# Performance work log

Measured on AMD Instinct MI355X. Metric: run time of the kernel, lower is better.

The kernel has to match this reference:

```python
import jax, jax.numpy as jnp
import numpy as np

POS_THRES = 0.7
NEG_THRES = 0.3
POS_RATIO = 0.5
N_SAMPLES = 256
FH, FW, STRIDE = 200, 200, 16
RATIOS = (1.0, 2.0)
N_GT = 256
IMG_H = FH * STRIDE
IMG_W = FW * STRIDE
A = FH * FW * len(RATIOS)
N_POS_BUDGET = int(POS_RATIO * N_SAMPLES)


def _make_anchors():
    # centre format [cy, cx, h, w]; one anchor per (cell, ratio)
    ys = (np.arange(FH) + 0.5) * STRIDE
    xs = (np.arange(FW) + 0.5) * STRIDE
    cy, cx = np.meshgrid(ys, xs, indexing='ij')          # [FH, FW]
    hs = np.array([STRIDE * np.sqrt(r) for r in RATIOS])  # [R]
    ws = np.array([STRIDE / np.sqrt(r) for r in RATIOS])
    cy = np.broadcast_to(cy[..., None], (FH, FW, len(RATIOS)))
    cx = np.broadcast_to(cx[..., None], (FH, FW, len(RATIOS)))
    h = np.broadcast_to(hs, (FH, FW, len(RATIOS)))
    w = np.broadcast_to(ws, (FH, FW, len(RATIOS)))
    centre = np.stack([cy, cx, h, w], -1).reshape(-1, 4).astype(np.float32)
    corner = np.stack([centre[:, 0] - centre[:, 2] / 2,
                       centre[:, 1] - centre[:, 3] / 2,
                       centre[:, 0] + centre[:, 2] / 2,
                       centre[:, 1] + centre[:, 3] / 2], -1).astype(np.float32)
    return jnp.asarray(centre), jnp.asarray(corner)


def setup_inputs() -> dict:
    key = jax.random.key(0)
    k1, k2, k3, k4, k5, k6 = jax.random.split(key, 6)
    centre_anchors, corner_anchors = _make_anchors()
    rpn_pred_bnd = jax.random.normal(k1, (1, A, 4), dtype=jnp.float32)
    rpn_pred_class = jax.random.normal(k2, (1, A, 2), dtype=jnp.float32)
    # gt boxes in centre form [cy, cx, h, w], inside the 3200x3200 image
    cy = jax.random.uniform(k3, (N_GT,), minval=200.0, maxval=IMG_H - 200.0)
    cx = jax.random.uniform(k4, (N_GT,), minval=200.0, maxval=IMG_W - 200.0)
    h = jax.random.uniform(k5, (N_GT,), minval=16.0, maxval=300.0)
    w = jax.random.uniform(k6, (N_GT,), minval=16.0, maxval=300.0)
    target_bnds = jnp.stack([cy, cx, h, w], 1).astype(jnp.float32)
    return {"rpn_pred_bnd": rpn_pred_bnd, "rpn_pred_class": rpn_pred_class,
            "target_bnds": target_bnds, "centre_anchors": centre_anchors,
            "corner_anchors": corner_anchors}


def _cxcy_to_corners(b):
    return jnp.stack([b[:, 0] - b[:, 2] / 2, b[:, 1] - b[:, 3] / 2,
                      b[:, 0] + b[:, 2] / 2, b[:, 1] + b[:, 3] / 2], 1)


def _iou(anc, tgt):
    # anc [A,4], tgt [N,4] in corner form [y1,x1,y2,x2] -> IoU [A,N]
    y1 = jnp.maximum(anc[:, None, 0], tgt[None, :, 0])
    x1 = jnp.maximum(anc[:, None, 1], tgt[None, :, 1])
    y2 = jnp.minimum(anc[:, None, 2], tgt[None, :, 2])
    x2 = jnp.minimum(anc[:, None, 3], tgt[None, :, 3])
    inter = jnp.clip(y2 - y1, 0.0) * jnp.clip(x2 - x1, 0.0)
    area_a = (anc[:, 2] - anc[:, 0]) * (anc[:, 3] - anc[:, 1])
    area_t = (tgt[:, 2] - tgt[:, 0]) * (tgt[:, 3] - tgt[:, 1])
    return inter / (area_a[:, None] + area_t[None, :] - inter)


def _subsample(mask, budget, key):
    # keep at most `budget` True entries, chosen uniformly at random (masked rank trick)
    pri = jax.random.uniform(key, mask.shape)
    pri = jnp.where(mask, pri, jnp.inf)
    order = jnp.argsort(pri)
    rank = jnp.zeros(mask.shape[0], dtype=jnp.int32).at[order].set(
        jnp.arange(mask.shape[0], dtype=jnp.int32))
    return mask & (rank < budget)


def reference(rpn_pred_bnd, rpn_pred_class, target_bnds, centre_anchors, corner_anchors):
    skey = jax.random.key(42)
    k_pos, k_neg = jax.random.split(skey)

    corner_targets = _cxcy_to_corners(target_bnds)
    valid = ((corner_anchors[:, 0] >= 0) & (corner_anchors[:, 1] >= 0) &
             (corner_anchors[:, 2] <= IMG_H) & (corner_anchors[:, 3] <= IMG_W))

    iou = _iou(corner_anchors, corner_targets)               # [A, N]
    iou = jnp.where(valid[:, None], iou, -1.0)               # mask invalid anchors out
    anchor_gt_overlap = iou.max(axis=1)                      # best gt per anchor
    anchor_gt_ind = iou.argmax(axis=1)
    gt_best_anchor = iou.argmax(axis=0)                      # best anchor per gt [N]

    labels = jnp.full((A,), -1, dtype=jnp.int32)
    labels = jnp.where(valid & (anchor_gt_overlap < NEG_THRES), 0, labels)
    labels = jnp.where(valid & (anchor_gt_overlap > POS_THRES), 1, labels)
    labels = labels.at[gt_best_anchor].set(1)                # force a positive per gt

    # subsample positives to POS_RATIO * N_SAMPLES
    keep_pos = _subsample(labels == 1, jnp.int32(N_POS_BUDGET), k_pos)
    labels = jnp.where((labels == 1) & ~keep_pos, -1, labels)
    n_pos_kept = jnp.sum(labels == 1).astype(jnp.int32)
    # subsample negatives to fill remaining budget
    keep_neg = _subsample(labels == 0, N_SAMPLES - n_pos_kept, k_neg)
    labels = jnp.where((labels == 0) & ~keep_neg, -1, labels)

    t = target_bnds[anchor_gt_ind]                           # [A,4]
    ty = (t[:, 0] - centre_anchors[:, 0]) / centre_anchors[:, 2]
    tx = (t[:, 1] - centre_anchors[:, 1]) / centre_anchors[:, 3]
    th = jnp.log(t[:, 2] / centre_anchors[:, 2])
    tw = jnp.log(t[:, 3] / centre_anchors[:, 3])
    anchor_targets = jnp.stack([ty, tx, th, tw], 1)

    pb = rpn_pred_bnd[0]                                     # [A,4]
    pc = rpn_pred_class[0]                                   # [A,2]
    posf = (labels == 1).astype(pb.dtype)
    negf = (labels == 0).astype(pb.dtype)
    n_pos = posf.sum()
    n_neg = negf.sum()

    def l1(c):
        return (jnp.abs(pb[:, c] - anchor_targets[:, c]) * posf).sum() / n_pos

    loss_y, loss_x, loss_h, loss_w = l1(0), l1(1), l1(2), l1(3)
    logp = jax.nn.log_softmax(pc, axis=-1)
    loss_pos_class = -(logp[:, 1] * posf).sum() / n_pos
    loss_neg_class = -(logp[:, 0] * negf).sum() / n_neg
    return (loss_x, loss_y, loss_h, loss_w, loss_pos_class, loss_neg_class)
```

## Files before the change

### kernel.cpp

```cpp
#include <hip/hip_runtime.h>
#include <stdint.h>

#pragma clang fp contract(off)

#define A_TOT   80000
#define NGT     256
#define IMGH    3200.0f
#define IMGW    3200.0f
#define NPOSB   128
#define NSAMP   256
#define FW      200
#define NBX     13
#define ANB     157
#define SEGW    512
#define NEG_BIN_MAX 119u
#define SENT (~0ull)
#define SELT 1024
#define SLOTS 16
#define SUBCAP 1024

struct U2 { uint32_t a, b; };

constexpr uint32_t rotl32c(uint32_t x, int d) {
  return (x << d) | (x >> (32 - d));
}

constexpr U2 tf2x32c(uint32_t k0, uint32_t k1, uint32_t x0, uint32_t x1) {
  uint32_t ks2 = k0 ^ k1 ^ 0x1BD11BDAu;
  x0 += k0; x1 += k1;
#define TF_G(r0_, r1_, r2_, r3_)                                   \
  { x0 += x1; x1 = rotl32c(x1, r0_); x1 ^= x0;                     \
    x0 += x1; x1 = rotl32c(x1, r1_); x1 ^= x0;                     \
    x0 += x1; x1 = rotl32c(x1, r2_); x1 ^= x0;                     \
    x0 += x1; x1 = rotl32c(x1, r3_); x1 ^= x0; }
  TF_G(13, 15, 26, 6);  x0 += k1;  x1 += ks2 + 1u;
  TF_G(17, 29, 16, 24); x0 += ks2; x1 += k0 + 2u;
  TF_G(13, 15, 26, 6);  x0 += k0;  x1 += k1 + 3u;
  TF_G(17, 29, 16, 24); x0 += k1;  x1 += ks2 + 4u;
  TF_G(13, 15, 26, 6);  x0 += ks2; x1 += k0 + 5u;
#undef TF_G
  return U2{x0, x1};
}

constexpr U2 KPOS = tf2x32c(0u, 42u, 0u, 0u);
constexpr U2 KNEG = tf2x32c(0u, 42u, 0u, 1u);

__device__ __forceinline__ uint32_t unif_prib(uint32_t k0, uint32_t k1, uint32_t idx) {
  U2 r = tf2x32c(k0, k1, 0u, idx);
  uint32_t w = r.a ^ r.b;
  uint32_t fb = (w >> 9) | 0x3f800000u;
  float pri = __uint_as_float(fb) - 1.0f;
  return __float_as_uint(pri);
}

__device__ __forceinline__ uint32_t binP(uint32_t pbv) {
  float pri = __uint_as_float(pbv);
  uint32_t b = (uint32_t)(pri * 512.0f);
  return b > 511u ? 511u : b;
}
__device__ __forceinline__ uint32_t binN(uint32_t pbv) {
  float pri = __uint_as_float(pbv);
  uint32_t b = (uint32_t)(pri * 65536.0f);
  return b > 511u ? 511u : b;
}

__device__ __forceinline__ float iou_fn(float ay1, float ax1, float ay2, float ax2,
                                        float area_a,
                                        float ty1, float tx1, float ty2, float tx2,
                                        float area_t) {
  float y1 = fmaxf(ay1, ty1);
  float x1 = fmaxf(ax1, tx1);
  float y2 = fminf(ay2, ty2);
  float x2 = fminf(ax2, tx2);
  float ih = y2 - y1; ih = fmaxf(ih, 0.0f);
  float iw = x2 - x1; iw = fmaxf(iw, 0.0f);
  float inter = ih * iw;
  float denom = area_a + area_t - inter;
  return inter / denom;
}

__device__ __forceinline__ uint32_t ord_bits(float v) {
  uint32_t b = __float_as_uint(v);
  return b ^ (((int)b < 0) ? 0xFFFFFFFFu : 0x80000000u);
}

__global__ __launch_bounds__(256)
void k_main(const float* __restrict__ cA, const float* __restrict__ tgt,
            int* __restrict__ labels, int* __restrict__ ind,
            uint32_t* __restrict__ gbest,
            unsigned long long* __restrict__ posSeg,
            unsigned long long* __restrict__ negSeg,
            uint32_t* __restrict__ posCntG, uint32_t* __restrict__ negCntG,
            uint32_t* __restrict__ negTotG) {
  int tid = threadIdx.x;
  int lane = tid & 63, wid = tid >> 6;
  if (blockIdx.x >= ANB) {
    int gt = blockIdx.x - ANB;
    float t0 = tgt[4*gt], t1 = tgt[4*gt+1], t2 = tgt[4*gt+2], t3 = tgt[4*gt+3];
    float ty1 = t0 - t2/2.0f, tx1 = t1 - t3/2.0f;
    float ty2 = t0 + t2/2.0f, tx2 = t1 + t3/2.0f;
    float at = (ty2 - ty1) * (tx2 - tx1);
    const float M = 11.5f;
    int iy0 = (int)floorf((ty1 - M) * 0.0625f - 0.5f) - 1; iy0 = iy0 < 0 ? 0 : iy0;
    int iy1 = (int)ceilf ((ty2 + M) * 0.0625f - 0.5f) + 1; iy1 = iy1 > 199 ? 199 : iy1;
    int ix0 = (int)floorf((tx1 - M) * 0.0625f - 0.5f) - 1; ix0 = ix0 < 0 ? 0 : ix0;
    int ix1 = (int)ceilf ((tx2 + M) * 0.0625f - 0.5f) + 1; ix1 = ix1 > 199 ? 199 : ix1;
    int wx = ix1 - ix0 + 1, wy = iy1 - iy0 + 1;
    int W = wy * wx * 2;
    unsigned long long key = 0ull;
    for (int c = tid; c < W; c += 256) {
      int r = c & 1, q = c >> 1;
      int yy = q / wx, xx = q - yy * wx;
      int a = (((iy0 + yy) * FW + (ix0 + xx)) << 1) | r;
      const float4 av = *reinterpret_cast<const float4*>(&cA[4*a]);
      float ay1 = av.x, ax1 = av.y, ay2 = av.z, ax2 = av.w;
      bool valid = (ay1 >= 0.f) & (ax1 >= 0.f) & (ay2 <= IMGH) & (ax2 <= IMGW);
      float v = -1.0f;
      if (valid) {
        float area_a = (ay2 - ay1) * (ax2 - ax1);
        v = iou_fn(ay1, ax1, ay2, ax2, area_a, ty1, tx1, ty2, tx2, at);
      }
      unsigned long long k2 =
          ((unsigned long long)ord_bits(v) << 32) | (uint32_t)(~(uint32_t)a);
      if (k2 > key) key = k2;
    }
    for (int d = 1; d < 64; d <<= 1) {
      unsigned long long o = __shfl_xor(key, d);
      if (o > key) key = o;
    }
    __shared__ unsigned long long sW[4];
    if (lane == 0) sW[wid] = key;
    __syncthreads();
    if (tid == 0) {
      unsigned long long k = sW[0];
      if (sW[1] > k) k = sW[1];
      if (sW[2] > k) k = sW[2];
      if (sW[3] > k) k = sW[3];
      gbest[gt] = ~(uint32_t)(k & 0xffffffffu);
    }
    return;
  }
  __shared__ float sTy1[NGT], sTx1[NGT], sTy2[NGT], sTx2[NGT], sAr[NGT];
  __shared__ uint32_t sCnt[256], sScan[256], sWs[4], sCur[176], sOrder[NGT];
  __shared__ uint32_t sPosCnt, sNegCnt, sNegTot;
  if (tid == 0) { sPosCnt = 0u; sNegCnt = 0u; sNegTot = 0u; }
  float t0 = tgt[4*tid], t1 = tgt[4*tid+1], t2 = tgt[4*tid+2], t3 = tgt[4*tid+3];
  float gy1 = t0 - t2/2.0f, gx1 = t1 - t3/2.0f;
  float gy2 = t0 + t2/2.0f, gx2 = t1 + t3/2.0f;
  sTy1[tid] = gy1; sTx1[tid] = gx1; sTy2[tid] = gy2; sTx2[tid] = gx2;
  sAr[tid] = (gy2 - gy1) * (gx2 - gx1);
  int gby = (int)(t0 * (1.0f/256.0f)); gby = gby > 12 ? 12 : gby;
  int gbx = (int)(t1 * (1.0f/256.0f)); gbx = gbx > 12 ? 12 : gbx;
  int gb = gby * NBX + gbx;
  sCnt[tid] = 0u;
  __syncthreads();
  atomicAdd(&sCnt[gb], 1u);
  __syncthreads();
  {
    uint32_t incl = sCnt[tid];
#pragma unroll
    for (int d = 1; d < 64; d <<= 1) {
      uint32_t o = __shfl_up(incl, d);
      if (lane >= d) incl += o;
    }
    if (lane == 63) sWs[wid] = incl;
    __syncthreads();
    uint32_t off = 0;
    if (wid > 0) off += sWs[0];
    if (wid > 1) off += sWs[1];
    if (wid > 2) off += sWs[2];
    sScan[tid] = incl + off;
  }
  __syncthreads();
  if (tid < 169) sCur[tid] = (tid == 0) ? 0u : sScan[tid - 1];
  __syncthreads();
  uint32_t pos = atomicAdd(&sCur[gb], 1u);
  sOrder[pos] = (uint32_t)tid;
  __syncthreads();
  int b = blockIdx.x;
#pragma unroll
  for (int half = 0; half < 2; half++) {
    int a = b * 512 + half * 256 + tid;
    int lab = -1;
    if (a < A_TOT) {
      const float4 av = *reinterpret_cast<const float4*>(&cA[4*a]);
      float ay1 = av.x, ax1 = av.y, ay2 = av.z, ax2 = av.w;
      bool valid = (ay1 >= 0.f) & (ax1 >= 0.f) & (ay2 <= IMGH) & (ax2 <= IMGW);
      float best = 0.0f; int bi = 0;
      if (valid) {
        float area_a = (ay2 - ay1) * (ax2 - ax1);
        int cell = a >> 1;
        int iy = cell / FW, ix = cell - iy * FW;
        int by = iy >> 4, bx = ix >> 4;
        int by0 = by > 0 ? by - 1 : 0, by1 = by < 12 ? by + 1 : 12;
        int bx0 = bx > 0 ? bx - 1 : 0, bx1 = bx < 12 ? bx + 1 : 12;
        for (int yy = by0; yy <= by1; yy++) {
          int rb = yy * NBX;
          int k0 = (rb + bx0 == 0) ? 0 : (int)sScan[rb + bx0 - 1];
          int k1 = (int)sScan[rb + bx1];
          for (int k = k0; k < k1; k++) {
            int g = (int)sOrder[k];
            float v = iou_fn(ay1, ax1, ay2, ax2, area_a,
                             sTy1[g], sTx1[g], sTy2[g], sTx2[g], sAr[g]);
            if (v > best || (v == best && g < bi)) { best = v; bi = g; }
          }
        }
        lab = (best < 0.3f) ? 0 : ((best > 0.7f) ? 1 : -1);
      }
      labels[a] = lab;
      ind[a] = bi;
      if (lab == 1) {
        uint32_t pbv = unif_prib(KPOS.a, KPOS.b, (uint32_t)a);
        uint32_t slot = atomicAdd(&sPosCnt, 1u);
        posSeg[b * SEGW + slot] = ((unsigned long long)pbv << 32) | (uint32_t)a;
      } else if (lab == 0) {
        uint32_t pbv = unif_prib(KNEG.a, KNEG.b, (uint32_t)a);
        if ((pbv >> 23) <= NEG_BIN_MAX) {
          uint32_t slot = atomicAdd(&sNegCnt, 1u);
          negSeg[b * SEGW + slot] = ((unsigned long long)pbv << 32) | (uint32_t)a;
        }
      }
    }
    unsigned long long mT = __ballot(lab == 0);
    if (lane == 0 && mT) atomicAdd(&sNegTot, (uint32_t)__popcll(mT));
  }
  __syncthreads();
  if (tid == 0) {
    posCntG[b] = sPosCnt; negCntG[b] = sNegCnt; negTotG[b] = sNegTot;
  }
}

__global__ __launch_bounds__(SELT)
void k_selloss(const float* __restrict__ pb, const float* __restrict__ pc,
               const float* __restrict__ tgt, const float* __restrict__ cAc,
               const int* __restrict__ labels, const int* __restrict__ ind,
               const uint32_t* __restrict__ gbest,
               const unsigned long long* __restrict__ posSeg,
               const unsigned long long* __restrict__ negSeg,
               const uint32_t* __restrict__ posCntG,
               const uint32_t* __restrict__ negCntG,
               const uint32_t* __restrict__ negTotG,
               float* __restrict__ out) {
  __shared__ uint32_t sFbit[2500];
  __shared__ uint32_t sG[NGT];
  __shared__ unsigned long long sFN[NGT];
  __shared__ uint32_t sPc[160], sNc[160];
  __shared__ uint32_t histP[512], histN[512];
  __shared__ __align__(16) unsigned long long sSubP[SUBCAP + 8];
  __shared__ __align__(16) unsigned long long sSubN[SUBCAP + 8];
  __shared__ uint32_t sTot[4];
  __shared__ uint32_t sNF, sNegRemoved, sSubPCnt, sSubNCnt, sBpos, sBneg;
  __shared__ float posC[NPOSB][5];
  __shared__ float negC[NSAMP];
  __shared__ float sWred[16];
  int tid = threadIdx.x;
  int lane = tid & 63;

  for (int i = tid; i < 2500; i += SELT) sFbit[i] = 0u;
  if (tid < 512) { histP[tid] = 0u; histN[tid] = 0u; }
  if (tid < NPOSB) {
    posC[tid][0] = posC[tid][1] = posC[tid][2] = posC[tid][3] = posC[tid][4] = 0.f;
  }
  if (tid < NSAMP) negC[tid] = 0.f;
  if (tid == 0) { sNF = 0u; sNegRemoved = 0u; sSubPCnt = 0u; sSubNCnt = 0u; }
  if (tid < 160) {
    sPc[tid] = (tid < ANB) ? posCntG[tid] : 0u;
    sNc[tid] = (tid < ANB) ? negCntG[tid] : 0u;
  }
  if (tid < NGT) sG[tid] = gbest[tid];
  __syncthreads();
  if (tid < 64) {
    uint32_t s = 0;
    for (int k = tid; k < ANB; k += 64) s += sPc[k];
#pragma unroll
    for (int d = 1; d < 64; d <<= 1) s += __shfl_xor(s, d);
    if (tid == 0) sTot[0] = s;
  } else if (tid < 128) {
    int l = tid - 64;
    uint32_t s = 0;
    for (int k = l; k < ANB; k += 64) s += negTotG[k];
#pragma unroll
    for (int d = 1; d < 64; d <<= 1) s += __shfl_xor(s, d);
    if (l == 0) sTot[2] = s;
  }
  __syncthreads();
  if (tid < NGT) {
    uint32_t a = sG[tid];
    uint32_t dup = 0;
#pragma unroll 8
    for (int j = 0; j < NGT; j++) dup |= (j < tid) & (sG[j] == a);
    if (!dup) {
      int lab = labels[a];
      if (lab != 1) {
        uint32_t pbv = unif_prib(KPOS.a, KPOS.b, a);
        uint32_t slot = atomicAdd(&sNF, 1u);
        sFN[slot] = ((unsigned long long)pbv << 32) | a;
      }
      if (lab == 0) {
        atomicOr(&sFbit[a >> 5], 1u << (a & 31));
        atomicAdd(&sNegRemoved, 1u);
      }
    }
  }
  __syncthreads();
  uint32_t P0 = sTot[0], negTotal = sTot[2], nF = sNF;
  uint32_t P = P0 + nF;
  uint32_t npk = P > NPOSB ? NPOSB : P;
  uint32_t budget = NSAMP - npk;
  uint32_t usableNeg = negTotal - sNegRemoved;
  bool negRank = (usableNeg >= budget);

  for (uint32_t idx = tid; idx < ANB * SLOTS; idx += SELT) {
    uint32_t bb = idx >> 4, k = idx & (SLOTS - 1);
    if (k < sPc[bb]) {
      unsigned long long key = posSeg[bb * SEGW + k];
      atomicAdd(&histP[binP((uint32_t)(key >> 32))], 1u);
    }
    if (k < sNc[bb]) {
      unsigned long long key = negSeg[bb * SEGW + k];
      uint32_t a = (uint32_t)(key & 0xffffffffu);
      if (!((sFbit[a >> 5] >> (a & 31)) & 1u))
        atomicAdd(&histN[binN((uint32_t)(key >> 32))], 1u);
    }
  }
  for (uint32_t bb = tid; bb < ANB; bb += SELT) {
    for (uint32_t k = SLOTS; k < sPc[bb]; k++) {
      unsigned long long key = posSeg[bb * SEGW + k];
      atomicAdd(&histP[binP((uint32_t)(key >> 32))], 1u);
    }
    for (uint32_t k = SLOTS; k < sNc[bb]; k++) {
      unsigned long long key = negSeg[bb * SEGW + k];
      uint32_t a = (uint32_t)(key & 0xffffffffu);
      if (!((sFbit[a >> 5] >> (a & 31)) & 1u))
        atomicAdd(&histN[binN((uint32_t)(key >> 32))], 1u);
    }
  }
  if (tid < nF)
    atomicAdd(&histP[binP((uint32_t)(sFN[tid] >> 32))], 1u);
  __syncthreads();
  if (tid < 64) {
    int base = tid * 8;
    uint32_t c[8], s = 0;
#pragma unroll
    for (int k = 0; k < 8; k++) { c[k] = histP[base + k]; s += c[k]; }
    uint32_t incl = s;
#pragma unroll
    for (int d = 1; d < 64; d <<= 1) {
      uint32_t o = __shfl_up(incl, d);
      if (tid >= d) incl += o;
    }
    uint32_t run = incl - s;
    int myB = 512;
#pragma unroll
    for (int k = 0; k < 8; k++) {
      run += c[k];
      if (run >= NPOSB && myB == 512) myB = base + k;
    }
#pragma unroll
    for (int d = 1; d < 64; d <<= 1) {
      int o = __shfl_xor(myB, d);
      if (o < myB) myB = o;
    }
    if (tid == 0) sBpos = (uint32_t)myB;
  } else if (tid < 128) {
    int l = tid - 64, base = l * 8;
    uint32_t c[8], s = 0;
#pragma unroll
    for (int k = 0; k < 8; k++) { c[k] = histN[base + k]; s += c[k]; }
    uint32_t incl = s;
#pragma unroll
    for (int d = 1; d < 64; d <<= 1) {
      uint32_t o = __shfl_up(incl, d);
      if (l >= d) incl += o;
    }
    uint32_t run = incl - s;
    int myB = 512;
#pragma unroll
    for (int k = 0; k < 8; k++) {
      run += c[k];
      if (run >= budget && myB == 512) myB = base + k;
    }
#pragma unroll
    for (int d = 1; d < 64; d <<= 1) {
      int o = __shfl_xor(myB, d);
      if (o < myB) myB = o;
    }
    if (l == 0) sBneg = (uint32_t)myB;
  }
  __syncthreads();
  uint32_t Bpos = sBpos, Bneg = sBneg;
  for (uint32_t idx = tid; idx < ANB * SLOTS; idx += SELT) {
    uint32_t bb = idx >> 4, k = idx & (SLOTS - 1);
    if (k < sPc[bb]) {
      unsigned long long key = posSeg[bb * SEGW + k];
      if (binP((uint32_t)(key >> 32)) <= Bpos) {
        uint32_t slot = atomicAdd(&sSubPCnt, 1u);
        if (slot < SUBCAP) sSubP[slot] = key;
      }
    }
    if (negRank && k < sNc[bb]) {
      unsigned long long key = negSeg[bb * SEGW + k];
      uint32_t a = (uint32_t)(key & 0xffffffffu);
      if (!((sFbit[a >> 5] >> (a & 31)) & 1u) &&
          binN((uint32_t)(key >> 32)) <= Bneg) {
        uint32_t slot = atomicAdd(&sSubNCnt, 1u);
        if (slot < SUBCAP) sSubN[slot] = key;
      }
    }
  }
  for (uint32_t bb = tid; bb < ANB; bb += SELT) {
    for (uint32_t k = SLOTS; k < sPc[bb]; k++) {
      unsigned long long key = posSeg[bb * SEGW + k];
      if (binP((uint32_t)(key >> 32)) <= Bpos) {
        uint32_t slot = atomicAdd(&sSubPCnt, 1u);
        if (slot < SUBCAP) sSubP[slot] = key;
      }
    }
    if (negRank) for (uint32_t k = SLOTS; k < sNc[bb]; k++) {
      unsigned long long key = negSeg[bb * SEGW + k];
      uint32_t a = (uint32_t)(key & 0xffffffffu);
      if (!((sFbit[a >> 5] >> (a & 31)) & 1u) &&
          binN((uint32_t)(key >> 32)) <= Bneg) {
        uint32_t slot = atomicAdd(&sSubNCnt, 1u);
        if (slot < SUBCAP) sSubN[slot] = key;
      }
    }
  }
  if (tid < nF) {
    unsigned long long key = sFN[tid];
    if (binP((uint32_t)(key >> 32)) <= Bpos) {
      uint32_t slot = atomicAdd(&sSubPCnt, 1u);
      if (slot < SUBCAP) sSubP[slot] = key;
    }
  }
  __syncthreads();
  uint32_t SP = sSubPCnt > SUBCAP ? SUBCAP : sSubPCnt;
  uint32_t SN = sSubNCnt > SUBCAP ? SUBCAP : sSubNCnt;
  uint32_t SPp = (SP + 7u) & ~7u;
  uint32_t SNp = (SN + 7u) & ~7u;
  for (uint32_t i = SP + tid; i < SPp; i += SELT) sSubP[i] = SENT;
  for (uint32_t i = SN + tid; i < SNp; i += SELT) sSubN[i] = SENT;
  __syncthreads();

  if ((uint32_t)(tid & ~63) < SP) {
    unsigned long long me = (tid < (int)SP) ? sSubP[tid] : SENT;
    uint32_t rk = 0;
    for (uint32_t j = 0; j < SPp; j += 8) {
      ulonglong2 v01 = *reinterpret_cast<const ulonglong2*>(&sSubP[j]);
      ulonglong2 v23 = *reinterpret_cast<const ulonglong2*>(&sSubP[j + 2]);
      ulonglong2 v45 = *reinterpret_cast<const ulonglong2*>(&sSubP[j + 4]);
      ulonglong2 v67 = *reinterpret_cast<const ulonglong2*>(&sSubP[j + 6]);
      rk += (v01.x < me) ? 1u : 0u;
      rk += (v01.y < me) ? 1u : 0u;
      rk += (v23.x < me) ? 1u : 0u;
      rk += (v23.y < me) ? 1u : 0u;
      rk += (v45.x < me) ? 1u : 0u;
      rk += (v45.y < me) ? 1u : 0u;
      rk += (v67.x < me) ? 1u : 0u;
      rk += (v67.y < me) ? 1u : 0u;
    }
    if (tid < (int)SP && rk < NPOSB) {
      uint32_t a = (uint32_t)(me & 0xffffffffu);
      const float* t = tgt + 4 * ind[a];
      float c0 = cAc[4*a], c1 = cAc[4*a+1], c2 = cAc[4*a+2], c3 = cAc[4*a+3];
      float ty = (t[0] - c0) / c2, tx = (t[1] - c1) / c3;
      float th = logf(t[2] / c2),  tw = logf(t[3] / c3);
      float q0 = pc[2*a], q1 = pc[2*a+1];
      float m = fmaxf(q0, q1);
      float l = logf(expf(q0 - m) + expf(q1 - m));
      posC[rk][0] = fabsf(pb[4*a+1] - tx);
      posC[rk][1] = fabsf(pb[4*a]   - ty);
      posC[rk][2] = fabsf(pb[4*a+2] - th);
      posC[rk][3] = fabsf(pb[4*a+3] - tw);
      posC[rk][4] = l - (q1 - m);
    }
  }

  if (negRank) {
    if ((uint32_t)(tid & ~63) < SN) {
      unsigned long long me = (tid < (int)SN) ? sSubN[tid] : SENT;
      uint32_t rk = 0;
      for (uint32_t j = 0; j < SNp; j += 8) {
        ulonglong2 v01 = *reinterpret_cast<const ulonglong2*>(&sSubN[j]);
        ulonglong2 v23 = *reinterpret_cast<const ulonglong2*>(&sSubN[j + 2]);
        ulonglong2 v45 = *reinterpret_cast<const ulonglong2*>(&sSubN[j + 4]);
        ulonglong2 v67 = *reinterpret_cast<const ulonglong2*>(&sSubN[j + 6]);
        rk += (v01.x < me) ? 1u : 0u;
        rk += (v01.y < me) ? 1u : 0u;
        rk += (v23.x < me) ? 1u : 0u;
        rk += (v23.y < me) ? 1u : 0u;
        rk += (v45.x < me) ? 1u : 0u;
        rk += (v45.y < me) ? 1u : 0u;
        rk += (v67.x < me) ? 1u : 0u;
        rk += (v67.y < me) ? 1u : 0u;
      }
      if (tid < (int)SN && rk < budget) {
        uint32_t a = (uint32_t)(me & 0xffffffffu);
        float q0 = pc[2*a], q1 = pc[2*a+1];
        float m = fmaxf(q0, q1);
        float l = logf(expf(q0 - m) + expf(q1 - m));
        negC[rk] = l - (q0 - m);
      }
    }
  } else {
    float acc = 0.f;
    for (int a = tid; a < A_TOT; a += SELT) {
      if (labels[a] == 0 && !((sFbit[a >> 5] >> (a & 31)) & 1u)) {
        float q0 = pc[2*a], q1 = pc[2*a+1];
        float m = fmaxf(q0, q1);
        float l = logf(expf(q0 - m) + expf(q1 - m));
        acc += l - (q0 - m);
      }
    }
    for (int d = 1; d < 64; d <<= 1) acc += __shfl_xor(acc, d);
    if (lane == 0) sWred[tid >> 6] = acc;
    __syncthreads();
    if (tid == 0) {
      float s = 0.f;
      for (int w = 0; w < 16; w++) s += sWred[w];
      negC[0] = s;
    }
  }
  __syncthreads();
  for (int s = 64; s >= 1; s >>= 1) {
    for (int r = tid; r < s; r += SELT)
      for (int k = 0; k < 5; k++) posC[r][k] += posC[r + s][k];
    __syncthreads();
  }
  for (int s = 128; s >= 1; s >>= 1) {
    for (int r = tid; r < s; r += SELT) negC[r] += negC[r + s];
    __syncthreads();
  }
  if (tid == 0) {
    float np = (float)npk;
    float nn = negRank ? (float)budget : (float)usableNeg;
    out[0] = posC[0][0] / np;
    out[1] = posC[0][1] / np;
    out[2] = posC[0][2] / np;
    out[3] = posC[0][3] / np;
    out[4] = posC[0][4] / np;
    out[5] = negC[0] / nn;
  }
}

extern "C" void kernel_launch(void* const* d_in, const int* in_sizes, int n_in,
                              void* d_out, int out_size, void* d_ws, size_t ws_size,
                              hipStream_t stream) {
  const float* rpn_pred_bnd   = (const float*)d_in[0];
  const float* rpn_pred_class = (const float*)d_in[1];
  const float* target_bnds    = (const float*)d_in[2];
  const float* centre_anchors = (const float*)d_in[3];
  const float* corner_anchors = (const float*)d_in[4];
  float* out = (float*)d_out;

  char* w = (char*)d_ws;
  size_t off = 0;
  auto carve = [&](size_t bytes) {
    void* p = w + off;
    off = (off + bytes + 255) & ~(size_t)255;
    return p;
  };
  uint32_t* gbest   = (uint32_t*)carve(NGT * sizeof(uint32_t));
  int*      labels  = (int*)carve(A_TOT * sizeof(int));
  int*      ind     = (int*)carve(A_TOT * sizeof(int));
  uint32_t* posCntG = (uint32_t*)carve(ANB * sizeof(uint32_t));
  uint32_t* negCntG = (uint32_t*)carve(ANB * sizeof(uint32_t));
  uint32_t* negTotG = (uint32_t*)carve(ANB * sizeof(uint32_t));
  unsigned long long* posSeg = (unsigned long long*)carve((size_t)ANB * SEGW * 8);
  unsigned long long* negSeg = (unsigned long long*)carve((size_t)ANB * SEGW * 8);
  (void)ws_size; (void)in_sizes; (void)n_in; (void)out_size;

  k_main<<<ANB + NGT, 256, 0, stream>>>(corner_anchors, target_bnds,
                                        labels, ind, gbest, posSeg, negSeg,
                                        posCntG, negCntG, negTotG);
  k_selloss<<<1, SELT, 0, stream>>>(rpn_pred_bnd, rpn_pred_class, target_bnds,
                                    centre_anchors, labels, ind, gbest,
                                    posSeg, negSeg, posCntG, negCntG, negTotG,
                                    out);
}
```

Before: 36.95 us.

## Replace per-block candidate segments with global atomic-compacted lists

The main kernel now appends positive and negative candidate keys to two compact global lists through global atomic counters, replacing per-block segments with per-block counts. The single-block selection kernel can then scan contiguous lists instead of walking 157 segments with a two-phase slot loop and reducing per-block counts. In exchange it adds global atomics contended across blocks, a memset launch to zero the counters, a fixed list capacity that silently truncates overflow, and a smaller shared sub-buffer capacity.

```diff
diff --git a/kernel.cpp b/kernel.cpp
--- a/kernel.cpp
+++ b/kernel.cpp
@@ -12,12 +12,11 @@
 #define FW      200
 #define NBX     13
 #define ANB     157
-#define SEGW    512
 #define NEG_BIN_MAX 119u
+#define LCAP    4096
 #define SENT (~0ull)
 #define SELT 1024
-#define SLOTS 16
-#define SUBCAP 1024
+#define SUBCAP 768
 
 struct U2 { uint32_t a, b; };
 
@@ -88,10 +87,9 @@
 void k_main(const float* __restrict__ cA, const float* __restrict__ tgt,
             int* __restrict__ labels, int* __restrict__ ind,
             uint32_t* __restrict__ gbest,
-            unsigned long long* __restrict__ posSeg,
-            unsigned long long* __restrict__ negSeg,
-            uint32_t* __restrict__ posCntG, uint32_t* __restrict__ negCntG,
-            uint32_t* __restrict__ negTotG) {
+            unsigned long long* __restrict__ posList,
+            unsigned long long* __restrict__ negList,
+            uint32_t* __restrict__ ctr) {
   int tid = threadIdx.x;
   int lane = tid & 63, wid = tid >> 6;
   if (blockIdx.x >= ANB) {
@@ -142,8 +140,8 @@
   }
   __shared__ float sTy1[NGT], sTx1[NGT], sTy2[NGT], sTx2[NGT], sAr[NGT];
   __shared__ uint32_t sCnt[256], sScan[256], sWs[4], sCur[176], sOrder[NGT];
-  __shared__ uint32_t sPosCnt, sNegCnt, sNegTot;
-  if (tid == 0) { sPosCnt = 0u; sNegCnt = 0u; sNegTot = 0u; }
+  __shared__ uint32_t sNegTot;
+  if (tid == 0) sNegTot = 0u;
   float t0 = tgt[4*tid], t1 = tgt[4*tid+1], t2 = tgt[4*tid+2], t3 = tgt[4*tid+3];
   float gy1 = t0 - t2/2.0f, gx1 = t1 - t3/2.0f;
   float gy2 = t0 + t2/2.0f, gx2 = t1 + t3/2.0f;
@@ -211,13 +209,13 @@
       ind[a] = bi;
       if (lab == 1) {
         uint32_t pbv = unif_prib(KPOS.a, KPOS.b, (uint32_t)a);
-        uint32_t slot = atomicAdd(&sPosCnt, 1u);
-        posSeg[b * SEGW + slot] = ((unsigned long long)pbv << 32) | (uint32_t)a;
+        uint32_t p = atomicAdd(&ctr[0], 1u);
+        if (p < LCAP) posList[p] = ((unsigned long long)pbv << 32) | (uint32_t)a;
       } else if (lab == 0) {
         uint32_t pbv = unif_prib(KNEG.a, KNEG.b, (uint32_t)a);
         if ((pbv >> 23) <= NEG_BIN_MAX) {
-          uint32_t slot = atomicAdd(&sNegCnt, 1u);
-          negSeg[b * SEGW + slot] = ((unsigned long long)pbv << 32) | (uint32_t)a;
+          uint32_t p = atomicAdd(&ctr[1], 1u);
+          if (p < LCAP) negList[p] = ((unsigned long long)pbv << 32) | (uint32_t)a;
         }
       }
     }
@@ -225,9 +223,7 @@
     if (lane == 0 && mT) atomicAdd(&sNegTot, (uint32_t)__popcll(mT));
   }
   __syncthreads();
-  if (tid == 0) {
-    posCntG[b] = sPosCnt; negCntG[b] = sNegCnt; negTotG[b] = sNegTot;
-  }
+  if (tid == 0 && sNegTot) atomicAdd(&ctr[2], sNegTot);
 }
 
 __global__ __launch_bounds__(SELT)
@@ -235,20 +231,17 @@
                const float* __restrict__ tgt, const float* __restrict__ cAc,
                const int* __restrict__ labels, const int* __restrict__ ind,
                const uint32_t* __restrict__ gbest,
-               const unsigned long long* __restrict__ posSeg,
-               const unsigned long long* __restrict__ negSeg,
-               const uint32_t* __restrict__ posCntG,
-               const uint32_t* __restrict__ negCntG,
-               const uint32_t* __restrict__ negTotG,
+               const unsigned long long* __restrict__ posList,
+               const unsigned long long* __restrict__ negList,
+               const uint32_t* __restrict__ ctr,
                float* __restrict__ out) {
   __shared__ uint32_t sFbit[2500];
   __shared__ uint32_t sG[NGT];
   __shared__ unsigned long long sFN[NGT];
-  __shared__ uint32_t sPc[160], sNc[160];
   __shared__ uint32_t histP[512], histN[512];
   __shared__ __align__(16) unsigned long long sSubP[SUBCAP + 8];
   __shared__ __align__(16) unsigned long long sSubN[SUBCAP + 8];
-  __shared__ uint32_t sTot[4];
+  __shared__ uint32_t sCtr[4];
   __shared__ uint32_t sNF, sNegRemoved, sSubPCnt, sSubNCnt, sBpos, sBneg;
   __shared__ float posC[NPOSB][5];
   __shared__ float negC[NSAMP];
@@ -263,27 +256,12 @@
   }
   if (tid < NSAMP) negC[tid] = 0.f;
   if (tid == 0) { sNF = 0u; sNegRemoved = 0u; sSubPCnt = 0u; sSubNCnt = 0u; }
-  if (tid < 160) {
-    sPc[tid] = (tid < ANB) ? posCntG[tid] : 0u;
-    sNc[tid] = (tid < ANB) ? negCntG[tid] : 0u;
-  }
+  if (tid < 4) sCtr[tid] = ctr[tid];
   if (tid < NGT) sG[tid] = gbest[tid];
   __syncthreads();
-  if (tid < 64) {
-    uint32_t s = 0;
-    for (int k = tid; k < ANB; k += 64) s += sPc[k];
-#pragma unroll
-    for (int d = 1; d < 64; d <<= 1) s += __shfl_xor(s, d);
-    if (tid == 0) sTot[0] = s;
-  } else if (tid < 128) {
-    int l = tid - 64;
-    uint32_t s = 0;
-    for (int k = l; k < ANB; k += 64) s += negTotG[k];
-#pragma unroll
-    for (int d = 1; d < 64; d <<= 1) s += __shfl_xor(s, d);
-    if (l == 0) sTot[2] = s;
-  }
-  __syncthreads();
+  uint32_t P0 = sCtr[0]; if (P0 > LCAP) P0 = LCAP;
+  uint32_t C0 = sCtr[1]; if (C0 > LCAP) C0 = LCAP;
+  uint32_t negTotal = sCtr[2];
   if (tid < NGT) {
     uint32_t a = sG[tid];
     uint32_t dup = 0;
@@ -303,40 +281,23 @@
     }
   }
   __syncthreads();
-  uint32_t P0 = sTot[0], negTotal = sTot[2], nF = sNF;
+  uint32_t nF = sNF;
   uint32_t P = P0 + nF;
   uint32_t npk = P > NPOSB ? NPOSB : P;
   uint32_t budget = NSAMP - npk;
   uint32_t usableNeg = negTotal - sNegRemoved;
   bool negRank = (usableNeg >= budget);
 
-  for (uint32_t idx = tid; idx < ANB * SLOTS; idx += SELT) {
-    uint32_t bb = idx >> 4, k = idx & (SLOTS - 1);
-    if (k < sPc[bb]) {
-      unsigned long long key = posSeg[bb * SEGW + k];
-      atomicAdd(&histP[binP((uint32_t)(key >> 32))], 1u);
-    }
-    if (k < sNc[bb]) {
-      unsigned long long key = negSeg[bb * SEGW + k];
-      uint32_t a = (uint32_t)(key & 0xffffffffu);
-      if (!((sFbit[a >> 5] >> (a & 31)) & 1u))
-        atomicAdd(&histN[binN((uint32_t)(key >> 32))], 1u);
-    }
-  }
-  for (uint32_t bb = tid; bb < ANB; bb += SELT) {
-    for (uint32_t k = SLOTS; k < sPc[bb]; k++) {
-      unsigned long long key = posSeg[bb * SEGW + k];
-      atomicAdd(&histP[binP((uint32_t)(key >> 32))], 1u);
-    }
-    for (uint32_t k = SLOTS; k < sNc[bb]; k++) {
-      unsigned long long key = negSeg[bb * SEGW + k];
-      uint32_t a = (uint32_t)(key & 0xffffffffu);
-      if (!((sFbit[a >> 5] >> (a & 31)) & 1u))
-        atomicAdd(&histN[binN((uint32_t)(key >> 32))], 1u);
-    }
-  }
+  for (uint32_t i = tid; i < P0; i += SELT)
+    atomicAdd(&histP[binP((uint32_t)(posList[i] >> 32))], 1u);
   if (tid < nF)
     atomicAdd(&histP[binP((uint32_t)(sFN[tid] >> 32))], 1u);
+  for (uint32_t i = tid; i < C0; i += SELT) {
+    unsigned long long key = negList[i];
+    uint32_t a = (uint32_t)(key & 0xffffffffu);
+    if (!((sFbit[a >> 5] >> (a & 31)) & 1u))
+      atomicAdd(&histN[binN((uint32_t)(key >> 32))], 1u);
+  }
   __syncthreads();
   if (tid < 64) {
     int base = tid * 8;
@@ -389,48 +350,29 @@
   }
   __syncthreads();
   uint32_t Bpos = sBpos, Bneg = sBneg;
-  for (uint32_t idx = tid; idx < ANB * SLOTS; idx += SELT) {
-    uint32_t bb = idx >> 4, k = idx & (SLOTS - 1);
-    if (k < sPc[bb]) {
-      unsigned long long key = posSeg[bb * SEGW + k];
-      if (binP((uint32_t)(key >> 32)) <= Bpos) {
-        uint32_t slot = atomicAdd(&sSubPCnt, 1u);
-        if (slot < SUBCAP) sSubP[slot] = key;
-      }
-    }
-    if (negRank && k < sNc[bb]) {
-      unsigned long long key = negSeg[bb * SEGW + k];
+  for (uint32_t i = tid; i < P0; i += SELT) {
+    unsigned long long key = posList[i];
+    if (binP((uint32_t)(key >> 32)) <= Bpos) {
+      uint32_t slot = atomicAdd(&sSubPCnt, 1u);
+      if (slot < SUBCAP) sSubP[slot] = key;
+    }
+  }
+  if (tid < nF) {
+    unsigned long long key = sFN[tid];
+    if (binP((uint32_t)(key >> 32)) <= Bpos) {
+      uint32_t slot = atomicAdd(&sSubPCnt, 1u);
+      if (slot < SUBCAP) sSubP[slot] = key;
+    }
+  }
+  if (negRank) {
+    for (uint32_t i = tid; i < C0; i += SELT) {
+      unsigned long long key = negList[i];
       uint32_t a = (uint32_t)(key & 0xffffffffu);
       if (!((sFbit[a >> 5] >> (a & 31)) & 1u) &&
           binN((uint32_t)(key >> 32)) <= Bneg) {
         uint32_t slot = atomicAdd(&sSubNCnt, 1u);
         if (slot < SUBCAP) sSubN[slot] = key;
       }
-    }
-  }
-  for (uint32_t bb = tid; bb < ANB; bb += SELT) {
-    for (uint32_t k = SLOTS; k < sPc[bb]; k++) {
-      unsigned long long key = posSeg[bb * SEGW + k];
-      if (binP((uint32_t)(key >> 32)) <= Bpos) {
-        uint32_t slot = atomicAdd(&sSubPCnt, 1u);
-        if (slot < SUBCAP) sSubP[slot] = key;
-      }
-    }
-    if (negRank) for (uint32_t k = SLOTS; k < sNc[bb]; k++) {
-      unsigned long long key = negSeg[bb * SEGW + k];
-      uint32_t a = (uint32_t)(key & 0xffffffffu);
-      if (!((sFbit[a >> 5] >> (a & 31)) & 1u) &&
-          binN((uint32_t)(key >> 32)) <= Bneg) {
-        uint32_t slot = atomicAdd(&sSubNCnt, 1u);
-        if (slot < SUBCAP) sSubN[slot] = key;
-      }
-    }
-  }
-  if (tid < nF) {
-    unsigned long long key = sFN[tid];
-    if (binP((uint32_t)(key >> 32)) <= Bpos) {
-      uint32_t slot = atomicAdd(&sSubPCnt, 1u);
-      if (slot < SUBCAP) sSubP[slot] = key;
     }
   }
   __syncthreads();
@@ -560,21 +502,18 @@
     off = (off + bytes + 255) & ~(size_t)255;
     return p;
   };
+  uint32_t* ctr     = (uint32_t*)carve(16 * sizeof(uint32_t));
   uint32_t* gbest   = (uint32_t*)carve(NGT * sizeof(uint32_t));
   int*      labels  = (int*)carve(A_TOT * sizeof(int));
   int*      ind     = (int*)carve(A_TOT * sizeof(int));
-  uint32_t* posCntG = (uint32_t*)carve(ANB * sizeof(uint32_t));
-  uint32_t* negCntG = (uint32_t*)carve(ANB * sizeof(uint32_t));
-  uint32_t* negTotG = (uint32_t*)carve(ANB * sizeof(uint32_t));
-  unsigned long long* posSeg = (unsigned long long*)carve((size_t)ANB * SEGW * 8);
-  unsigned long long* negSeg = (unsigned long long*)carve((size_t)ANB * SEGW * 8);
+  unsigned long long* posList = (unsigned long long*)carve(LCAP * 8);
+  unsigned long long* negList = (unsigned long long*)carve(LCAP * 8);
   (void)ws_size; (void)in_sizes; (void)n_in; (void)out_size;
 
+  hipMemsetAsync(ctr, 0, 16 * sizeof(uint32_t), stream);
   k_main<<<ANB + NGT, 256, 0, stream>>>(corner_anchors, target_bnds,
-                                        labels, ind, gbest, posSeg, negSeg,
-                                        posCntG, negCntG, negTotG);
+                                        labels, ind, gbest, posList, negList, ctr);
   k_selloss<<<1, SELT, 0, stream>>>(rpn_pred_bnd, rpn_pred_class, target_bnds,
                                     centre_anchors, labels, ind, gbest,
-                                    posSeg, negSeg, posCntG, negCntG, negTotG,
-                                    out);
-}
+                                    posList, negList, ctr, out);
+}
```

New measurement: 38.76 us. +4.9%, slower.
